# Kernel tuning notes

Measured on AMD Instinct MI355X. Metric: run time of the kernel, lower is better.

Reference implementation:

```python
import jax, jax.numpy as jnp
import numpy as np

B = 64          # batch
LS = 1024       # Nt * N
LW = 1024       # beamformer length
LY = 2048       # measurement length
M = 16          # number of sensors
N_STEP = 10     # unrolled update steps
MODULUS = 1.0
D = 2 * LS + 2 * LW + LY   # 6144, MLP input dim
H = 512                    # MLP hidden dim


def setup_inputs() -> dict:
    key = jax.random.key(0)
    ks = jax.random.split(key, 18)
    r = lambda k, shp, s: jax.random.normal(k, shp, dtype=jnp.float32) * s
    W_SCALE = 0.02  # keep the unrolled recursion numerically stable
    return {
        "phi0_batch": jax.random.uniform(ks[0], (B, LS), dtype=jnp.float32,
                                         minval=-np.pi, maxval=np.pi),
        "w_M_re": r(ks[1], (B, LW, M), 1.0),
        "w_M_im": r(ks[2], (B, LW, M), 1.0),
        "y_M": r(ks[3], (LY, M), 1.0),
        # est_eta_modules: D -> H -> LS
        "eW1": r(ks[4], (D, H), W_SCALE), "eb1": jnp.zeros((H,), jnp.float32),
        "eW2": r(ks[5], (H, LS), W_SCALE), "eb2": jnp.zeros((LS,), jnp.float32),
        # est_rho_modules: D -> H -> 1
        "rW1": r(ks[6], (D, H), W_SCALE), "rb1": jnp.zeros((H,), jnp.float32),
        "rW2": r(ks[7], (H, 1), W_SCALE), "rb2": jnp.zeros((1,), jnp.float32),
        # est_mu_modules: D -> H -> 1
        "mW1": r(ks[8], (D, H), W_SCALE), "mb1": jnp.zeros((H,), jnp.float32),
        "mW2": r(ks[9], (H, 1), W_SCALE), "mb2": jnp.zeros((1,), jnp.float32),
    }


def _mlp(x, W1, b1, W2, b2):
    return jax.nn.relu(x @ W1 + b1) @ W2 + b2


def _forward(phi0, w_re, w_im, y,
             eW1, eb1, eW2, eb2, rW1, rb1, rW2, rb2, mW1, mb1, mW2, mb2):
    # per-(batch, sensor) static features
    wr = jnp.swapaxes(w_re, 1, 2)                       # [B, M, LW]
    wi = jnp.swapaxes(w_im, 1, 2)                       # [B, M, LW]
    yt = jnp.broadcast_to(y.T[None], (phi0.shape[0], M, LY))  # [B, M, LY]

    def step(phi, _):
        s = MODULUS * jnp.exp(1j * phi)                 # [B, LS] complex64
        sr = jnp.broadcast_to(s.real[:, None, :], (phi.shape[0], M, LS))
        si = jnp.broadcast_to(s.imag[:, None, :], (phi.shape[0], M, LS))
        x = jnp.concatenate([sr, si, wr, wi, yt], axis=-1)  # [B, M, D]
        eta = _mlp(x, eW1, eb1, eW2, eb2)               # [B, M, LS]
        rho = _mlp(x, rW1, rb1, rW2, rb2)               # [B, M, 1]
        mu = _mlp(x, mW1, mb1, mW2, mb2)                # [B, M, 1]
        eta_net = jnp.sum(mu * rho * eta, axis=1)       # [B, LS]
        return phi - eta_net, s

    phi_f, s_seq = jax.lax.scan(step, phi0, None, length=N_STEP)
    s_last = MODULUS * jnp.exp(1j * phi_f)              # [B, LS]
    # [B, N_STEP+1, LS]
    return jnp.concatenate([jnp.moveaxis(s_seq, 0, 1), s_last[:, None, :]], axis=1)


def reference(phi0_batch, w_M_re, w_M_im, y_M,
              eW1, eb1, eW2, eb2, rW1, rb1, rW2, rb2, mW1, mb1, mW2, mb2):
    s_stack = _forward(phi0_batch, w_M_re, w_M_im, y_M,
                       eW1, eb1, eW2, eb2, rW1, rb1, rW2, rb2,
                       mW1, mb1, mW2, mb2)
    # complex output represented as stacked (real, imag): [B, N_STEP+1, LS, 2]
    s_ri = jnp.stack([s_stack.real, s_stack.imag], axis=-1)
    # faithful to original: mu_stack_batch is allocated but never written
    mu_stack = jnp.zeros((phi0_batch.shape[0], N_STEP, M), jnp.float32)
    return (s_ri, mu_stack)
```

## Files before the change

### kernel.cpp

```cpp
#include <hip/hip_runtime.h>
#include <math.h>

#define OFF_STAT  0u
#define SZ_STAT   (3u*1024u*512u)
#define OFF_PHI   (OFF_STAT + SZ_STAT)
#define SZ_PHI    (64u*1024u)
#define OFF_CS    (OFF_PHI + SZ_PHI)
#define SZ_CS     (64u*2048u)
#define OFF_SCR   (OFF_CS + SZ_CS)
#define OFF_AT    OFF_SCR
#define OFF_YPART (OFF_AT + 1024u*2048u)
#define OFF_YSTAT (OFF_YPART + 3u*8u*16u*512u)
#define OFF_DYNP  OFF_SCR
#define OFF_HW    (OFF_DYNP + 48u*64u*512u)
#define OFF_SUMC  (OFF_HW + 64u*512u)
#define OFF_ETAP  (OFF_SUMC + 64u)

#define OUT_S_FLOATS (64u*11u*1024u*2u)

__global__ __launch_bounds__(256) void k_transpose(
    const float* __restrict__ wre, const float* __restrict__ wim,
    float* __restrict__ AT) {
  __shared__ float tile[64][17];
  int b = blockIdx.x, l0 = blockIdx.y * 64;
  const float* src = blockIdx.z ? wim : wre;
  int koff = blockIdx.z ? 1024 : 0;
  {
    int i4 = threadIdx.x * 4;
    int l = i4 >> 4, m = i4 & 15;
    float4 v = *(const float4*)(src + ((size_t)b * 1024 + l0 + l) * 16 + m);
    tile[l][m] = v.x; tile[l][m + 1] = v.y; tile[l][m + 2] = v.z; tile[l][m + 3] = v.w;
  }
  __syncthreads();
  {
    int i4 = threadIdx.x * 4;
    int l = i4 & 63, m = i4 >> 6;
    float4 o;
    o.x = tile[l + 0][m]; o.y = tile[l + 1][m];
    o.z = tile[l + 2][m]; o.w = tile[l + 3][m];
    *(float4*)(AT + ((size_t)(b * 16 + m)) * 2048 + koff + l0 + l) = o;
  }
}

__global__ __launch_bounds__(512) void k_ystat_part(
    const float* __restrict__ y,
    const float* __restrict__ eW1, const float* __restrict__ rW1,
    const float* __restrict__ mW1, float* __restrict__ ypart) {
  int mlp = blockIdx.x, m = blockIdx.y, slab = blockIdx.z, h = threadIdx.x;
  const float* W1 = (mlp == 0) ? eW1 : (mlp == 1) ? rW1 : mW1;
  int k0 = slab * 256;
  const float* Wp = W1 + (size_t)(4096 + k0) * 512 + h;
  const float* yp = y + (size_t)k0 * 16 + m;
  float acc = 0.f;
  #pragma unroll 8
  for (int l = 0; l < 256; ++l)
    acc = fmaf(yp[l * 16], Wp[(size_t)l * 512], acc);
  ypart[(((size_t)mlp * 8 + slab) * 16 + m) * 512 + h] = acc;
}

__global__ __launch_bounds__(512) void k_ystat_red(
    const float* __restrict__ ypart,
    const float* __restrict__ eb1, const float* __restrict__ rb1,
    const float* __restrict__ mb1, float* __restrict__ ystat) {
  int mlp = blockIdx.x, m = blockIdx.y, h = threadIdx.x;
  const float* b1 = (mlp == 0) ? eb1 : (mlp == 1) ? rb1 : mb1;
  float acc = b1[h];
  #pragma unroll
  for (int s = 0; s < 8; ++s)
    acc += ypart[(((size_t)mlp * 8 + s) * 16 + m) * 512 + h];
  ystat[((size_t)mlp * 16 + m) * 512 + h] = acc;
}

__global__ __launch_bounds__(256) void k_static_gemm(
    const float* __restrict__ AT,
    const float* __restrict__ eW1, const float* __restrict__ rW1,
    const float* __restrict__ mW1,
    const float* __restrict__ ystat, float* __restrict__ stat) {
  int mlp = blockIdx.z;
  const float* W1 = (mlp == 0) ? eW1 : (mlp == 1) ? rW1 : mW1;
  int m0 = blockIdx.x * 32, n0 = blockIdx.y * 64;
  const float* Bbase = W1 + 2048u * 512u + n0;
  __shared__ float As[2][16][36];
  __shared__ float Bs[2][16][64];
  int tid = threadIdx.x;
  int ty = tid >> 4, tx = tid & 15;
  int arow = tid >> 3, akk = (tid & 7) << 1;
  int bkk = tid >> 4, bnn = (tid & 15) << 2;
  const float* Ap = AT + (size_t)(m0 + arow) * 2048 + akk;
  const float* Bp = Bbase + (size_t)bkk * 512 + bnn;
  float2 av = *(const float2*)(Ap);
  float4 bv = *(const float4*)(Bp);
  float acc[2][4] = {};
  int buf = 0;
  for (int k0 = 0; k0 < 2048; k0 += 16) {
    As[buf][akk][arow] = av.x; As[buf][akk + 1][arow] = av.y;
    *(float4*)&Bs[buf][bkk][bnn] = bv;
    __syncthreads();
    int kn = (k0 + 16 < 2048) ? k0 + 16 : k0;
    av = *(const float2*)(Ap + kn);
    bv = *(const float4*)(Bp + (size_t)kn * 512);
    #pragma unroll
    for (int k = 0; k < 16; ++k) {
      float2 a = *(const float2*)&As[buf][k][ty << 1];
      float4 bb = *(const float4*)&Bs[buf][k][tx << 2];
      float ar[2] = {a.x, a.y};
      float br[4] = {bb.x, bb.y, bb.z, bb.w};
      #pragma unroll
      for (int i = 0; i < 2; ++i)
        #pragma unroll
        for (int j = 0; j < 4; ++j)
          acc[i][j] = fmaf(ar[i], br[j], acc[i][j]);
    }
    buf ^= 1;
  }
  #pragma unroll
  for (int i = 0; i < 2; ++i) {
    int bm = m0 + (ty << 1) + i;
    const float* ys = ystat + ((size_t)mlp * 16 + (bm & 15)) * 512 + n0;
    float* cp = stat + ((size_t)mlp * 1024 + bm) * 512 + n0;
    #pragma unroll
    for (int j = 0; j < 4; ++j)
      cp[(tx << 2) + j] = acc[i][j] + ys[(tx << 2) + j];
  }
}

__global__ __launch_bounds__(256) void k_dyn(
    const float* __restrict__ A,
    const float* __restrict__ B0, const float* __restrict__ B1,
    const float* __restrict__ B2, float* __restrict__ C) {
  const float* Bm = (blockIdx.z == 0) ? B0 : (blockIdx.z == 1) ? B1 : B2;
  int n0 = blockIdx.x * 64;
  int kbase = blockIdx.y * 128;
  __shared__ float As[2][16][68];
  __shared__ float Bs[2][16][64];
  int tid = threadIdx.x;
  int ty = tid >> 4, tx = tid & 15;
  int arow = tid >> 2, akk = (tid & 3) << 2;
  int bkk = tid >> 4, bnn = (tid & 15) << 2;
  const float* Ap = A + (size_t)arow * 2048 + kbase + akk;
  const float* Bp = Bm + ((size_t)(kbase + bkk)) * 512 + n0 + bnn;
  float4 av = *(const float4*)(Ap);
  float4 bv = *(const float4*)(Bp);
  float acc[4][4] = {};
  int buf = 0;
  for (int k0 = 0; k0 < 128; k0 += 16) {
    As[buf][akk + 0][arow] = av.x; As[buf][akk + 1][arow] = av.y;
    As[buf][akk + 2][arow] = av.z; As[buf][akk + 3][arow] = av.w;
    *(float4*)&Bs[buf][bkk][bnn] = bv;
    __syncthreads();
    int kn = (k0 + 16 < 128) ? k0 + 16 : k0;
    av = *(const float4*)(Ap + kn);
    bv = *(const float4*)(Bp + (size_t)kn * 512);
    #pragma unroll
    for (int k = 0; k < 16; ++k) {
      float4 a = *(const float4*)&As[buf][k][ty << 2];
      float4 bb = *(const float4*)&Bs[buf][k][tx << 2];
      float ar[4] = {a.x, a.y, a.z, a.w};
      float br[4] = {bb.x, bb.y, bb.z, bb.w};
      #pragma unroll
      for (int i = 0; i < 4; ++i)
        #pragma unroll
        for (int j = 0; j < 4; ++j)
          acc[i][j] = fmaf(ar[i], br[j], acc[i][j]);
    }
    buf ^= 1;
  }
  int chunk = blockIdx.y * 3 + blockIdx.z;
  float* Cp = C + ((size_t)chunk * 64) * 512 + n0;
  #pragma unroll
  for (int i = 0; i < 4; ++i)
    #pragma unroll
    for (int j = 0; j < 4; ++j)
      Cp[((size_t)((ty << 2) + i)) * 512 + (tx << 2) + j] = acc[i][j];
}

__global__ __launch_bounds__(512) void k_reduce(
    const float* __restrict__ dynp, const float* __restrict__ stat,
    const float* __restrict__ rW2, const float* __restrict__ rb2,
    const float* __restrict__ mW2, const float* __restrict__ mb2,
    float* __restrict__ hw, float* __restrict__ sumc) {
  int b = blockIdx.x, h = threadIdx.x;
  float de = 0.f, dr = 0.f, dm = 0.f;
  #pragma unroll
  for (int s = 0; s < 16; ++s) {
    de += dynp[((size_t)((s * 3 + 0) * 64 + b)) * 512 + h];
    dr += dynp[((size_t)((s * 3 + 1) * 64 + b)) * 512 + h];
    dm += dynp[((size_t)((s * 3 + 2) * 64 + b)) * 512 + h];
  }
  float wr2 = rW2[h], wm2 = mW2[h];
  int lane = h & 63, wave = h >> 6;
  __shared__ float s_r[16][8], s_m[16][8], s_c[16];
  const float* se_p = stat + ((size_t)(0 * 1024) + b * 16) * 512 + h;
  const float* sr_p = stat + ((size_t)(1 * 1024) + b * 16) * 512 + h;
  const float* sm_p = stat + ((size_t)(2 * 1024) + b * 16) * 512 + h;
  float he[16];
  #pragma unroll
  for (int m = 0; m < 16; ++m) {
    he[m] = fmaxf(de + se_p[(size_t)m * 512], 0.f);
    float hr = fmaxf(dr + sr_p[(size_t)m * 512], 0.f);
    float hm = fmaxf(dm + sm_p[(size_t)m * 512], 0.f);
    float pr = hr * wr2, pm = hm * wm2;
    #pragma unroll
    for (int off = 32; off; off >>= 1) {
      pr += __shfl_down(pr, off);
      pm += __shfl_down(pm, off);
    }
    if (lane == 0) { s_r[m][wave] = pr; s_m[m][wave] = pm; }
  }
  __syncthreads();
  if (h < 16) {
    int m = h;
    float rho = rb2[0], mu = mb2[0];
    #pragma unroll
    for (int w = 0; w < 8; ++w) { rho += s_r[m][w]; mu += s_m[m][w]; }
    float coeff = rho * mu;
    s_c[m] = coeff;
    float t = coeff;
    #pragma unroll
    for (int off = 8; off; off >>= 1) t += __shfl_down(t, off);
    if (m == 0) sumc[b] = t;
  }
  __syncthreads();
  float hwacc = 0.f;
  #pragma unroll
  for (int m = 0; m < 16; ++m) hwacc = fmaf(s_c[m], he[m], hwacc);
  hw[(size_t)b * 512 + h] = hwacc;
}

__global__ __launch_bounds__(256) void k_etap(
    const float* __restrict__ hw, const float* __restrict__ eW2,
    float* __restrict__ etap) {
  int n0 = blockIdx.x * 64;
  int kbase = blockIdx.y * 64;
  __shared__ float As[2][16][68];
  __shared__ float Bs[2][16][64];
  int tid = threadIdx.x;
  int ty = tid >> 4, tx = tid & 15;
  int arow = tid >> 2, akk = (tid & 3) << 2;
  int bkk = tid >> 4, bnn = (tid & 15) << 2;
  const float* Ap = hw + (size_t)arow * 512 + kbase + akk;
  const float* Bp = eW2 + (size_t)(kbase + bkk) * 1024 + n0 + bnn;
  float4 av = *(const float4*)(Ap);
  float4 bv = *(const float4*)(Bp);
  float acc[4][4] = {};
  int buf = 0;
  for (int k0 = 0; k0 < 64; k0 += 16) {
    As[buf][akk + 0][arow] = av.x; As[buf][akk + 1][arow] = av.y;
    As[buf][akk + 2][arow] = av.z; As[buf][akk + 3][arow] = av.w;
    *(float4*)&Bs[buf][bkk][bnn] = bv;
    __syncthreads();
    int kn = (k0 + 16 < 64) ? k0 + 16 : k0;
    av = *(const float4*)(Ap + kn);
    bv = *(const float4*)(Bp + (size_t)kn * 1024);
    #pragma unroll
    for (int k = 0; k < 16; ++k) {
      float4 a = *(const float4*)&As[buf][k][ty << 2];
      float4 bb = *(const float4*)&Bs[buf][k][tx << 2];
      float ar[4] = {a.x, a.y, a.z, a.w};
      float br[4] = {bb.x, bb.y, bb.z, bb.w};
      #pragma unroll
      for (int i = 0; i < 4; ++i)
        #pragma unroll
        for (int j = 0; j < 4; ++j)
          acc[i][j] = fmaf(ar[i], br[j], acc[i][j]);
    }
    buf ^= 1;
  }
  float* Cp = etap + ((size_t)blockIdx.y * 64) * 1024 + n0;
  #pragma unroll
  for (int i = 0; i < 4; ++i)
    #pragma unroll
    for (int j = 0; j < 4; ++j)
      Cp[((size_t)((ty << 2) + i)) * 1024 + (tx << 2) + j] = acc[i][j];
}

__global__ __launch_bounds__(256) void k_update(
    const float* __restrict__ etap, const float* __restrict__ eb2,
    const float* __restrict__ sumc, float* __restrict__ phi,
    float* __restrict__ cs, float* __restrict__ out, int t) {
  int i = blockIdx.x * 256 + threadIdx.x;
  int b = i >> 10, k = i & 1023;
  float e = sumc[b] * eb2[k];
  #pragma unroll
  for (int s = 0; s < 8; ++s)
    e += etap[((size_t)(s * 64 + b)) * 1024 + k];
  float p = phi[i] - e;
  phi[i] = p;
  float sn, cn;
  sincosf(p, &sn, &cn);
  cs[(size_t)b * 2048 + k] = cn;
  cs[(size_t)b * 2048 + 1024 + k] = sn;
  size_t o = (((size_t)(b * 11 + t + 1)) * 1024 + k) * 2;
  out[o] = cn; out[o + 1] = sn;
}

__global__ __launch_bounds__(256) void k_init(
    const float* __restrict__ phi0, float* __restrict__ phi,
    float* __restrict__ cs, float* __restrict__ out) {
  int bid = blockIdx.x;
  if (bid < 256) {
    int i = bid * 256 + threadIdx.x;
    float p = phi0[i];
    phi[i] = p;
    int b = i >> 10, k = i & 1023;
    float sn, cn;
    sincosf(p, &sn, &cn);
    cs[(size_t)b * 2048 + k] = cn;
    cs[(size_t)b * 2048 + 1024 + k] = sn;
    size_t o = (((size_t)b * 11) * 1024 + k) * 2;
    out[o] = cn; out[o + 1] = sn;
  } else {
    int j = (bid - 256) * 256 + threadIdx.x;
    out[OUT_S_FLOATS + j] = 0.f;
  }
}

extern "C" void kernel_launch(void* const* d_in, const int* in_sizes, int n_in,
                              void* d_out, int out_size, void* d_ws, size_t ws_size,
                              hipStream_t stream) {
  const float* phi0 = (const float*)d_in[0];
  const float* wre  = (const float*)d_in[1];
  const float* wim  = (const float*)d_in[2];
  const float* y    = (const float*)d_in[3];
  const float* eW1  = (const float*)d_in[4];
  const float* eb1  = (const float*)d_in[5];
  const float* eW2  = (const float*)d_in[6];
  const float* eb2  = (const float*)d_in[7];
  const float* rW1  = (const float*)d_in[8];
  const float* rb1  = (const float*)d_in[9];
  const float* rW2  = (const float*)d_in[10];
  const float* rb2  = (const float*)d_in[11];
  const float* mW1  = (const float*)d_in[12];
  const float* mb1  = (const float*)d_in[13];
  const float* mW2  = (const float*)d_in[14];
  const float* mb2  = (const float*)d_in[15];

  float* ws    = (float*)d_ws;
  float* stat  = ws + OFF_STAT;
  float* phi   = ws + OFF_PHI;
  float* cs    = ws + OFF_CS;
  float* AT    = ws + OFF_AT;
  float* ypart = ws + OFF_YPART;
  float* ystat = ws + OFF_YSTAT;
  float* dynp  = ws + OFF_DYNP;
  float* hw    = ws + OFF_HW;
  float* sumc  = ws + OFF_SUMC;
  float* etap  = ws + OFF_ETAP;
  float* out   = (float*)d_out;

  k_transpose<<<dim3(64, 16, 2), dim3(256), 0, stream>>>(wre, wim, AT);
  k_ystat_part<<<dim3(3, 16, 8), dim3(512), 0, stream>>>(y, eW1, rW1, mW1, ypart);
  k_ystat_red<<<dim3(3, 16), dim3(512), 0, stream>>>(ypart, eb1, rb1, mb1, ystat);
  k_static_gemm<<<dim3(32, 8, 3), dim3(256), 0, stream>>>(AT, eW1, rW1, mW1, ystat, stat);
  k_init<<<dim3(296), dim3(256), 0, stream>>>(phi0, phi, cs, out);

  for (int t = 0; t < 10; ++t) {
    k_dyn<<<dim3(8, 16, 3), dim3(256), 0, stream>>>(cs, eW1, rW1, mW1, dynp);
    k_reduce<<<dim3(64), dim3(512), 0, stream>>>(
        dynp, stat, rW2, rb2, mW2, mb2, hw, sumc);
    k_etap<<<dim3(16, 8), dim3(256), 0, stream>>>(hw, eW2, etap);
    k_update<<<dim3(256), dim3(256), 0, stream>>>(
        etap, eb2, sumc, phi, cs, out, t);
  }
}
```

Measured before the change: 576.7 us.

## Fuse transpose into static GEMM, use larger tiles and split-K with reduction

```diff
diff --git a/kernel.cpp b/kernel.cpp
--- a/kernel.cpp
+++ b/kernel.cpp
@@ -1,46 +1,22 @@
 #include <hip/hip_runtime.h>
 #include <math.h>
 
-#define OFF_STAT  0u
-#define SZ_STAT   (3u*1024u*512u)
-#define OFF_PHI   (OFF_STAT + SZ_STAT)
-#define SZ_PHI    (64u*1024u)
-#define OFF_CS    (OFF_PHI + SZ_PHI)
-#define SZ_CS     (64u*2048u)
-#define OFF_SCR   (OFF_CS + SZ_CS)
-#define OFF_AT    OFF_SCR
-#define OFF_YPART (OFF_AT + 1024u*2048u)
-#define OFF_YSTAT (OFF_YPART + 3u*8u*16u*512u)
-#define OFF_DYNP  OFF_SCR
-#define OFF_HW    (OFF_DYNP + 48u*64u*512u)
-#define OFF_SUMC  (OFF_HW + 64u*512u)
-#define OFF_ETAP  (OFF_SUMC + 64u)
+#define OFF_PHI    0u
+#define SZ_PHI     (64u*1024u)
+#define OFF_CS     (OFF_PHI + SZ_PHI)
+#define SZ_CS      (64u*2048u)
+#define OFF_STAT   (OFF_CS + SZ_CS)
+#define SZ_STAT    (3u*1024u*512u)
+#define OFF_SCR    (OFF_STAT + SZ_STAT)
+#define OFF_STATP1 OFF_SCR
+#define OFF_YPART  (OFF_STATP1 + SZ_STAT)
+#define OFF_YSTAT  (OFF_YPART + 3u*8u*16u*512u)
+#define OFF_DYNP   OFF_SCR
+#define OFF_HW     (OFF_DYNP + 48u*64u*512u)
+#define OFF_SUMC   (OFF_HW + 64u*512u)
+#define OFF_ETAP   (OFF_SUMC + 64u)
 
 #define OUT_S_FLOATS (64u*11u*1024u*2u)
-
-__global__ __launch_bounds__(256) void k_transpose(
-    const float* __restrict__ wre, const float* __restrict__ wim,
-    float* __restrict__ AT) {
-  __shared__ float tile[64][17];
-  int b = blockIdx.x, l0 = blockIdx.y * 64;
-  const float* src = blockIdx.z ? wim : wre;
-  int koff = blockIdx.z ? 1024 : 0;
-  {
-    int i4 = threadIdx.x * 4;
-    int l = i4 >> 4, m = i4 & 15;
-    float4 v = *(const float4*)(src + ((size_t)b * 1024 + l0 + l) * 16 + m);
-    tile[l][m] = v.x; tile[l][m + 1] = v.y; tile[l][m + 2] = v.z; tile[l][m + 3] = v.w;
-  }
-  __syncthreads();
-  {
-    int i4 = threadIdx.x * 4;
-    int l = i4 & 63, m = i4 >> 6;
-    float4 o;
-    o.x = tile[l + 0][m]; o.y = tile[l + 1][m];
-    o.z = tile[l + 2][m]; o.w = tile[l + 3][m];
-    *(float4*)(AT + ((size_t)(b * 16 + m)) * 2048 + koff + l0 + l) = o;
-  }
-}
 
 __global__ __launch_bounds__(512) void k_ystat_part(
     const float* __restrict__ y,
@@ -72,56 +48,85 @@
 }
 
 __global__ __launch_bounds__(256) void k_static_gemm(
-    const float* __restrict__ AT,
+    const float* __restrict__ wre, const float* __restrict__ wim,
     const float* __restrict__ eW1, const float* __restrict__ rW1,
     const float* __restrict__ mW1,
-    const float* __restrict__ ystat, float* __restrict__ stat) {
-  int mlp = blockIdx.z;
+    float* __restrict__ statp0, float* __restrict__ statp1) {
+  int mlp = blockIdx.z >> 1, khalf = blockIdx.z & 1;
   const float* W1 = (mlp == 0) ? eW1 : (mlp == 1) ? rW1 : mW1;
-  int m0 = blockIdx.x * 32, n0 = blockIdx.y * 64;
-  const float* Bbase = W1 + 2048u * 512u + n0;
-  __shared__ float As[2][16][36];
-  __shared__ float Bs[2][16][64];
+  const float* src = khalf ? wim : wre;
+  int m0 = blockIdx.x * 64, n0 = blockIdx.y * 64;
+  int b0 = m0 >> 4;
+  const float* Bbase = W1 + (size_t)(2048 + 1024 * khalf) * 512 + n0;
+
+  __shared__ float As[2][32][68];
+  __shared__ float Bs[2][32][64];
   int tid = threadIdx.x;
   int ty = tid >> 4, tx = tid & 15;
-  int arow = tid >> 3, akk = (tid & 7) << 1;
-  int bkk = tid >> 4, bnn = (tid & 15) << 2;
-  const float* Ap = AT + (size_t)(m0 + arow) * 2048 + akk;
-  const float* Bp = Bbase + (size_t)bkk * 512 + bnn;
-  float2 av = *(const float2*)(Ap);
-  float4 bv = *(const float4*)(Bp);
-  float acc[2][4] = {};
+
+  int a_ab0 = tid >> 7, a_al = (tid >> 2) & 31, a_am4 = (tid & 3) << 2;
+  int b_br = tid >> 4, b_bn4 = (tid & 15) << 2;
+
+  const float* ApG0 = src + ((size_t)(b0 + a_ab0)     * 1024 + a_al) * 16 + a_am4;
+  const float* ApG1 = src + ((size_t)(b0 + a_ab0 + 2) * 1024 + a_al) * 16 + a_am4;
+  const float* BpG0 = Bbase + (size_t)b_br * 512 + b_bn4;
+  const float* BpG1 = Bbase + (size_t)(b_br + 16) * 512 + b_bn4;
+  float4 a0 = *(const float4*)(ApG0);
+  float4 a1 = *(const float4*)(ApG1);
+  float4 bv0 = *(const float4*)(BpG0);
+  float4 bv1 = *(const float4*)(BpG1);
+
+  float acc[4][4] = {};
   int buf = 0;
-  for (int k0 = 0; k0 < 2048; k0 += 16) {
-    As[buf][akk][arow] = av.x; As[buf][akk + 1][arow] = av.y;
-    *(float4*)&Bs[buf][bkk][bnn] = bv;
+  for (int kk = 0; kk < 1024; kk += 32) {
+    *(float4*)&As[buf][a_al][(a_ab0 << 4) + a_am4] = a0;
+    *(float4*)&As[buf][a_al][((a_ab0 + 2) << 4) + a_am4] = a1;
+    *(float4*)&Bs[buf][b_br][b_bn4] = bv0;
+    *(float4*)&Bs[buf][b_br + 16][b_bn4] = bv1;
     __syncthreads();
-    int kn = (k0 + 16 < 2048) ? k0 + 16 : k0;
-    av = *(const float2*)(Ap + kn);
-    bv = *(const float4*)(Bp + (size_t)kn * 512);
-    #pragma unroll
-    for (int k = 0; k < 16; ++k) {
-      float2 a = *(const float2*)&As[buf][k][ty << 1];
+    int kn = (kk + 32 < 1024) ? kk + 32 : kk;
+    a0 = *(const float4*)(ApG0 + (size_t)kn * 16);
+    a1 = *(const float4*)(ApG1 + (size_t)kn * 16);
+    bv0 = *(const float4*)(BpG0 + (size_t)kn * 512);
+    bv1 = *(const float4*)(BpG1 + (size_t)kn * 512);
+    #pragma unroll
+    for (int k = 0; k < 32; ++k) {
+      float4 a = *(const float4*)&As[buf][k][ty << 2];
       float4 bb = *(const float4*)&Bs[buf][k][tx << 2];
-      float ar[2] = {a.x, a.y};
+      float ar[4] = {a.x, a.y, a.z, a.w};
       float br[4] = {bb.x, bb.y, bb.z, bb.w};
       #pragma unroll
-      for (int i = 0; i < 2; ++i)
+      for (int i = 0; i < 4; ++i)
         #pragma unroll
         for (int j = 0; j < 4; ++j)
           acc[i][j] = fmaf(ar[i], br[j], acc[i][j]);
     }
     buf ^= 1;
   }
-  #pragma unroll
-  for (int i = 0; i < 2; ++i) {
-    int bm = m0 + (ty << 1) + i;
-    const float* ys = ystat + ((size_t)mlp * 16 + (bm & 15)) * 512 + n0;
-    float* cp = stat + ((size_t)mlp * 1024 + bm) * 512 + n0;
-    #pragma unroll
-    for (int j = 0; j < 4; ++j)
-      cp[(tx << 2) + j] = acc[i][j] + ys[(tx << 2) + j];
-  }
+  float* statp = khalf ? statp1 : statp0;
+  #pragma unroll
+  for (int i = 0; i < 4; ++i) {
+    int bm = m0 + (ty << 2) + i;
+    float* cp = statp + ((size_t)mlp * 1024 + bm) * 512 + n0 + (tx << 2);
+    #pragma unroll
+    for (int j = 0; j < 4; ++j) cp[j] = acc[i][j];
+  }
+}
+
+__global__ __launch_bounds__(256) void k_stat_red(
+    float* __restrict__ statp0, const float* __restrict__ statp1,
+    const float* __restrict__ ystat) {
+  unsigned f4 = blockIdx.x * 256 + threadIdx.x;
+  size_t flat = (size_t)f4 * 4;
+  unsigned mlp = flat >> 19;
+  unsigned rem = flat & ((1u << 19) - 1);
+  unsigned bm = rem >> 9, h = rem & 511;
+  float4 v0 = *(const float4*)(statp0 + flat);
+  float4 v1 = *(const float4*)(statp1 + flat);
+  float4 ys = *(const float4*)(ystat + ((size_t)mlp * 16 + (bm & 15)) * 512 + h);
+  v0.x += v1.x + ys.x; v0.y += v1.y + ys.y;
+  v0.z += v1.z + ys.z; v0.w += v1.w + ys.w;
+  *(float4*)(statp0 + flat) = v0;
 }
 
 __global__ __launch_bounds__(256) void k_dyn(
@@ -335,23 +340,24 @@
   const float* mW2  = (const float*)d_in[14];
   const float* mb2  = (const float*)d_in[15];
 
-  float* ws    = (float*)d_ws;
-  float* stat  = ws + OFF_STAT;
-  float* phi   = ws + OFF_PHI;
-  float* cs    = ws + OFF_CS;
-  float* AT    = ws + OFF_AT;
-  float* ypart = ws + OFF_YPART;
-  float* ystat = ws + OFF_YSTAT;
-  float* dynp  = ws + OFF_DYNP;
-  float* hw    = ws + OFF_HW;
-  float* sumc  = ws + OFF_SUMC;
-  float* etap  = ws + OFF_ETAP;
-  float* out   = (float*)d_out;
-
-  k_transpose<<<dim3(64, 16, 2), dim3(256), 0, stream>>>(wre, wim, AT);
+  float* ws     = (float*)d_ws;
+  float* phi    = ws + OFF_PHI;
+  float* cs     = ws + OFF_CS;
+  float* stat   = ws + OFF_STAT;
+  float* statp1 = ws + OFF_STATP1;
+  float* ypart  = ws + OFF_YPART;
+  float* ystat  = ws + OFF_YSTAT;
+  float* dynp   = ws + OFF_DYNP;
+  float* hw     = ws + OFF_HW;
+  float* sumc   = ws + OFF_SUMC;
+  float* etap   = ws + OFF_ETAP;
+  float* out    = (float*)d_out;
+
   k_ystat_part<<<dim3(3, 16, 8), dim3(512), 0, stream>>>(y, eW1, rW1, mW1, ypart);
   k_ystat_red<<<dim3(3, 16), dim3(512), 0, stream>>>(ypart, eb1, rb1, mb1, ystat);
-  k_static_gemm<<<dim3(32, 8, 3), dim3(256), 0, stream>>>(AT, eW1, rW1, mW1, ystat, stat);
+  k_static_gemm<<<dim3(16, 8, 6), dim3(256), 0, stream>>>(
+      wre, wim, eW1, rW1, mW1, stat, statp1);
+  k_stat_red<<<dim3(1536), dim3(256), 0, stream>>>(stat, statp1, ystat);
   k_init<<<dim3(296), dim3(256), 0, stream>>>(phi0, phi, cs, out);
 
   for (int t = 0; t < 10; ++t) {
```

Result: faster. 543.7 us (-5.7%).
